# Kernel tuning notes

Hardware: AMD Instinct MI355X
Metric: run time of the kernel (lower is better)

Reference implementation:

```python
import jax, jax.numpy as jnp
from jax import lax
import numpy as np

EPS = 1e-5
NEG_SLOPE = 0.1
POOL = 2


def _cond_block(x, w, b, fcw, fcb, g, be, rm, rv):
    """CondConv1d(k=3,pad=1,num_experts=e) + BatchNorm1d(eval) + LeakyReLU(0.1).
    x: (B, Cin, W); w: (E, Cout, Cin, 3); b: (E, Cout); fcw: (E, Cin); fcb: (E,)
    """
    # routing: adaptive avg pool to 1 -> fc -> sigmoid  => (B, E)
    r = jax.nn.sigmoid(x.mean(axis=-1) @ fcw.T + fcb)
    # per-sample mixed weights/bias
    cw = jnp.einsum('be,eoik->boik', r, w)          # (B, Cout, Cin, 3)
    cb = r @ b                                      # (B, Cout)
    # batched per-sample conv1d (same padding, stride 1)
    def one(xi, wi):
        return lax.conv_general_dilated(
            xi[None], wi, window_strides=(1,), padding=[(1, 1)],
            dimension_numbers=('NCH', 'OIH', 'NCH'))[0]
    y = jax.vmap(one)(x, cw) + cb[:, :, None]       # (B, Cout, W)
    # BatchNorm1d in eval mode (running stats)
    y = (y - rm[None, :, None]) * (g[None, :, None] / jnp.sqrt(rv[None, :, None] + EPS)) + be[None, :, None]
    # LeakyReLU(0.1)
    return jnp.where(y >= 0, y, NEG_SLOPE * y)


def setup_inputs() -> dict:
    key = jax.random.key(0)
    ks = jax.random.split(key, 16)
    B, W = 32, 2048
    chans = [64, 128, 256]
    E = 1  # num_experts default
    inp = {'x': jax.random.normal(ks[0], (B, chans[0], W), dtype=jnp.float32)}
    i = 1
    for li, (ci, co) in enumerate(zip(chans[:-1], chans[1:]), start=1):
        fan_in = ci * 3
        wb = float(np.sqrt(6.0 / fan_in))  # kaiming_uniform a=sqrt(5) scale approx
        bb = float(1.0 / np.sqrt(fan_in))
        inp[f'w{li}'] = jax.random.uniform(ks[i], (E, co, ci, 3), minval=-wb, maxval=wb, dtype=jnp.float32); i += 1
        inp[f'b{li}'] = jax.random.uniform(ks[i], (E, co), minval=-bb, maxval=bb, dtype=jnp.float32); i += 1
        inp[f'fcw{li}'] = jax.random.normal(ks[i], (E, ci), dtype=jnp.float32) * 0.05; i += 1
        inp[f'fcb{li}'] = jnp.zeros((E,), dtype=jnp.float32)
        inp[f'g{li}'] = 1.0 + 0.1 * jax.random.normal(ks[i], (co,), dtype=jnp.float32); i += 1
        inp[f'be{li}'] = 0.1 * jax.random.normal(ks[i], (co,), dtype=jnp.float32); i += 1
        inp[f'rm{li}'] = 0.1 * jax.random.normal(ks[i], (co,), dtype=jnp.float32); i += 1
        inp[f'rv{li}'] = 0.5 + jax.random.uniform(ks[i], (co,), dtype=jnp.float32); i += 1
    return inp


def reference(x, w1, b1, fcw1, fcb1, g1, be1, rm1, rv1,
              w2, b2, fcw2, fcb2, g2, be2, rm2, rv2):
    y = _cond_block(x, w1, b1, fcw1, fcb1, g1, be1, rm1, rv1)
    y = _cond_block(y, w2, b2, fcw2, fcb2, g2, be2, rm2, rv2)
    # max_pool1d(kernel=stride=POOL)
    B, C, W = y.shape
    y = y.reshape(B, C, W // POOL, POOL).max(axis=-1)
    # dropout: eval mode -> identity
    return y
```

## Files before the change

kernel.cpp:

```cpp
#include <hip/hip_runtime.h>
#include <hip/hip_bf16.h>
#include <math.h>

#define BATCH 32
#define WLEN  2048

typedef __attribute__((ext_vector_type(8))) short short8;
typedef __attribute__((ext_vector_type(4))) short short4v;
typedef __attribute__((ext_vector_type(4))) float floatx4;

__device__ inline short f2bf(float f) {
  unsigned u = __float_as_uint(f);
  unsigned r = (u + 0x7fffu + ((u >> 16) & 1u)) >> 16;
  return (short)r;
}

__global__ __launch_bounds__(256) void fused_prep(
    const float* __restrict__ w1, const float* __restrict__ w2,
    const float* __restrict__ x, const float* __restrict__ fcw1,
    short* __restrict__ wp1, short* __restrict__ wp2,
    float* __restrict__ racc1) {
  const int blk = blockIdx.x;
  const int tid = threadIdx.x;
  if (blk < 12) {
    int iw = blk * 256 + tid;
    int o = iw & 127;
    int t = iw >> 7;
    int ig = t & 7;
    int k = t >> 3;
    short8 v;
#pragma unroll
    for (int e = 0; e < 8; ++e) v[e] = f2bf(w1[(o * 64 + ig * 8 + e) * 3 + k]);
    *(short8*)(wp1 + (size_t)iw * 8) = v;
  } else if (blk < 60) {
    int iw = (blk - 12) * 256 + tid;
    int o = iw & 255;
    int t = iw >> 8;
    int ig = t & 15;
    int k = t >> 4;
    short8 v;
#pragma unroll
    for (int e = 0; e < 8; ++e) v[e] = f2bf(w2[(o * 128 + ig * 8 + e) * 3 + k]);
    *(short8*)(wp2 + (size_t)iw * 8) = v;
  } else {
    int t = blk - 60;
    int j = t & 7, b = t >> 3;
    const float4* xb = (const float4*)(x + ((size_t)b * 64 + j * 8) * WLEN);
    float sum = 0.f;
    for (int idx = tid; idx < 8 * 512; idx += 256) {
      int c = idx >> 9;
      float4 v = xb[idx];
      sum += (v.x + v.y + v.z + v.w) * fcw1[j * 8 + c];
    }
    __shared__ float red[256];
    red[tid] = sum;
    __syncthreads();
    for (int s = 128; s > 0; s >>= 1) {
      if (tid < s) red[tid] += red[tid + s];
      __syncthreads();
    }
    if (tid == 0) racc1[b * 8 + j] = red[0];
  }
}

__global__ __launch_bounds__(512, 4) void conv1_mfma(
    const float* __restrict__ x, const short* __restrict__ wp1,
    const float* __restrict__ bias, const float* __restrict__ g,
    const float* __restrict__ be, const float* __restrict__ rm,
    const float* __restrict__ rv, const float* __restrict__ racc1,
    const float* __restrict__ fcb, const float* __restrict__ fcw2,
    short* __restrict__ y1p, float* __restrict__ racc2) {
  const int b = blockIdx.y;
  const int w0 = blockIdx.x * 128;
  const int tid = threadIdx.x;
  const int wave = tid >> 6, lane = tid & 63;
  const int ln = lane & 15, kg = lane >> 4;
  const int oh = wave & 1, wq = wave >> 1;

  __shared__ short xs[8 * 130 * 8];
  __shared__ float red[512];

  const float* xb = x + (size_t)b * 64 * WLEN;
  for (int idx = tid; idx < 8 * 130; idx += 512) {
    int ig = idx / 130;
    int p = idx - ig * 130;
    int w = w0 - 1 + p;
    short8 v = {0, 0, 0, 0, 0, 0, 0, 0};
    if ((unsigned)w < (unsigned)WLEN) {
      const float* src = xb + (size_t)(ig * 8) * WLEN + w;
#pragma unroll
      for (int e = 0; e < 8; ++e) v[e] = f2bf(src[(size_t)e * WLEN]);
    }
    *(short8*)(xs + idx * 8) = v;
  }
  __syncthreads();

  floatx4 acc[4][2];
#pragma unroll
  for (int ms = 0; ms < 4; ++ms)
#pragma unroll
    for (int ns = 0; ns < 2; ++ns) acc[ms][ns] = (floatx4){0.f, 0.f, 0.f, 0.f};

#pragma unroll
  for (int q = 0; q < 2; ++q) {
#pragma unroll
    for (int k = 0; k < 3; ++k) {
      short8 af[4], bf[2];
      const short* wk =
          wp1 + ((size_t)(k * 8 + q * 4 + kg) * 128 + oh * 64 + ln) * 8;
#pragma unroll
      for (int ms = 0; ms < 4; ++ms)
        af[ms] = *(const short8*)(wk + (size_t)ms * 16 * 8);
#pragma unroll
      for (int ns = 0; ns < 2; ++ns)
        bf[ns] = *(const short8*)(
            xs + ((q * 4 + kg) * 130 + wq * 32 + ns * 16 + ln + k) * 8);
#pragma unroll
      for (int ms = 0; ms < 4; ++ms)
#pragma unroll
        for (int ns = 0; ns < 2; ++ns)
          acc[ms][ns] = __builtin_amdgcn_mfma_f32_16x16x32_bf16(
              af[ms], bf[ns], acc[ms][ns], 0, 0, 0);
    }
  }

  float zs = 0.f;
#pragma unroll
  for (int qq = 0; qq < 8; ++qq) zs += racc1[b * 8 + qq];
  float z = zs * (1.f / (float)WLEN) + fcb[0];
  float r1v = 1.f / (1.f + expf(-z));

  float rsum2 = 0.f;
#pragma unroll
  for (int ms = 0; ms < 4; ++ms) {
    const int o0 = oh * 64 + ms * 16 + kg * 4;
    float a_[4], c_[4], fw[4];
#pragma unroll
    for (int rr = 0; rr < 4; ++rr) {
      int o = o0 + rr;
      float s = g[o] * rsqrtf(rv[o] + 1e-5f);
      a_[rr] = r1v * s;
      c_[rr] = (r1v * bias[o] - rm[o]) * s + be[o];
      fw[rr] = fcw2[o];
    }
#pragma unroll
    for (int ns = 0; ns < 2; ++ns) {
      int w = w0 + wq * 32 + ns * 16 + ln;
      short pk[4];
#pragma unroll
      for (int rr = 0; rr < 4; ++rr) {
        float v = acc[ms][ns][rr] * a_[rr] + c_[rr];
        v = v >= 0.f ? v : 0.1f * v;
        rsum2 += v * fw[rr];
        pk[rr] = f2bf(v);
      }
      unsigned u0 = (unsigned)(unsigned short)pk[0] |
                    ((unsigned)(unsigned short)pk[1] << 16);
      unsigned u1 = (unsigned)(unsigned short)pk[2] |
                    ((unsigned)(unsigned short)pk[3] << 16);
      unsigned p0 = __shfl_xor((int)u0, 16);
      unsigned p1 = __shfl_xor((int)u1, 16);
      if (!(kg & 1)) {
        int4 s8;
        s8.x = (int)u0; s8.y = (int)u1; s8.z = (int)p0; s8.w = (int)p1;
        *(int4*)(y1p + ((size_t)(b * 16 + (o0 >> 3)) * WLEN + w) * 8) = s8;
      }
    }
  }
  red[tid] = rsum2;
  __syncthreads();
  for (int s = 256; s > 0; s >>= 1) {
    if (tid < s) red[tid] += red[tid + s];
    __syncthreads();
  }
  if (tid == 0) racc2[b * 16 + blockIdx.x] = red[0];
}

__global__ __launch_bounds__(256) void conv2_mfma(
    const short* __restrict__ y1p, const short* __restrict__ wp2,
    const float* __restrict__ bias, const float* __restrict__ g,
    const float* __restrict__ be, const float* __restrict__ rm,
    const float* __restrict__ rv, const float* __restrict__ racc2,
    const float* __restrict__ fcb, float* __restrict__ out) {
  const int b = blockIdx.y;
  const int w0 = blockIdx.x * 128;
  const int tid = threadIdx.x;
  const int oq = tid >> 6, lane = tid & 63;
  const int ln = lane & 15, kg = lane >> 4;

  __shared__ short xs[16 * 130 * 8];

  const short* yb = y1p + (size_t)b * 16 * WLEN * 8;
  for (int idx = tid; idx < 16 * 130; idx += 256) {
    int ig = idx / 130;
    int p = idx - ig * 130;
    int w = w0 - 1 + p;
    short8 v = {0, 0, 0, 0, 0, 0, 0, 0};
    if ((unsigned)w < (unsigned)WLEN)
      v = *(const short8*)(yb + ((size_t)ig * WLEN + w) * 8);
    *(short8*)(xs + idx * 8) = v;
  }
  __syncthreads();

  floatx4 acc[4][8];
#pragma unroll
  for (int ms = 0; ms < 4; ++ms)
#pragma unroll
    for (int ns = 0; ns < 8; ++ns) acc[ms][ns] = (floatx4){0.f, 0.f, 0.f, 0.f};

#pragma unroll
  for (int c = 0; c < 12; ++c) {
    const int q = c >> 2, kk = c & 3;
    const int qq = c / 3, k = c % 3;
    (void)q; (void)kk;

    short8 af[4], bf[8];
    const short* wk =
        wp2 + ((size_t)(k * 16 + qq * 4 + kg) * 256 + oq * 64 + ln) * 8;
#pragma unroll
    for (int ms = 0; ms < 4; ++ms)
      af[ms] = *(const short8*)(wk + (size_t)ms * 16 * 8);
#pragma unroll
    for (int ns = 0; ns < 8; ++ns)
      bf[ns] = *(const short8*)(
          xs + ((qq * 4 + kg) * 130 + ns * 16 + ln + k) * 8);
#pragma unroll
    for (int ms = 0; ms < 4; ++ms)
#pragma unroll
      for (int ns = 0; ns < 8; ++ns)
        acc[ms][ns] = __builtin_amdgcn_mfma_f32_16x16x32_bf16(
            af[ms], bf[ns], acc[ms][ns], 0, 0, 0);
  }

  float zs = 0.f;
#pragma unroll
  for (int t = 0; t < 16; ++t) zs += racc2[b * 16 + t];
  float z = zs * (1.f / (float)WLEN) + fcb[0];
  float r2v = 1.f / (1.f + expf(-z));

#pragma unroll
  for (int ms = 0; ms < 4; ++ms) {
    const int o0 = oq * 64 + ms * 16 + kg * 4;
    float a_[4], c_[4];
#pragma unroll
    for (int rr = 0; rr < 4; ++rr) {
      int o = o0 + rr;
      float s = g[o] * rsqrtf(rv[o] + 1e-5f);
      a_[rr] = r2v * s;
      c_[rr] = (r2v * bias[o] - rm[o]) * s + be[o];
    }
#pragma unroll
    for (int np = 0; np < 4; ++np) {
      float m0[4], m1[4];
#pragma unroll
      for (int half = 0; half < 2; ++half) {
        int ns = np * 2 + half;
#pragma unroll
        for (int rr = 0; rr < 4; ++rr) {
          float v = acc[ms][ns][rr] * a_[rr] + c_[rr];
          v = v >= 0.f ? v : 0.1f * v;
          float m = fmaxf(v, __shfl_xor(v, 1));
          if (half == 0) m0[rr] = m; else m1[rr] = m;
        }
      }
      const int pc = (w0 >> 1) + np * 16 + ln;
#pragma unroll
      for (int rr = 0; rr < 4; ++rr) {
        int src = kg * 16 + ((ln & 7) << 1);
        float aa = __shfl(m0[rr], src);
        float bb = __shfl(m1[rr], src);
        float val = (ln < 8) ? aa : bb;
        out[((size_t)(b * 256 + o0 + rr)) * (WLEN / 2) + pc] = val;
      }
    }
  }
}

extern "C" void kernel_launch(void* const* d_in, const int* in_sizes, int n_in,
                              void* d_out, int out_size, void* d_ws, size_t ws_size,
                              hipStream_t stream) {
  const float* x    = (const float*)d_in[0];
  const float* w1   = (const float*)d_in[1];
  const float* b1   = (const float*)d_in[2];
  const float* fcw1 = (const float*)d_in[3];
  const float* fcb1 = (const float*)d_in[4];
  const float* g1   = (const float*)d_in[5];
  const float* be1  = (const float*)d_in[6];
  const float* rm1  = (const float*)d_in[7];
  const float* rv1  = (const float*)d_in[8];
  const float* w2   = (const float*)d_in[9];
  const float* b2   = (const float*)d_in[10];
  const float* fcw2 = (const float*)d_in[11];
  const float* fcb2 = (const float*)d_in[12];
  const float* g2   = (const float*)d_in[13];
  const float* be2  = (const float*)d_in[14];
  const float* rm2  = (const float*)d_in[15];
  const float* rv2  = (const float*)d_in[16];
  float* out = (float*)d_out;

  char* ws = (char*)d_ws;
  short* y1p   = (short*)ws;
  short* wp1   = (short*)(ws + (size_t)16 * 1024 * 1024);
  short* wp2   = (short*)(ws + (size_t)16 * 1024 * 1024 + 65536);
  float* racc1 = (float*)(ws + (size_t)16 * 1024 * 1024 + 327680);
  float* racc2 = racc1 + 256;

  fused_prep<<<316, 256, 0, stream>>>(w1, w2, x, fcw1, wp1, wp2, racc1);
  conv1_mfma<<<dim3(16, 32), 512, 0, stream>>>(
      x, wp1, b1, g1, be1, rm1, rv1, racc1, fcb1, fcw2, y1p, racc2);
  conv2_mfma<<<dim3(16, 32), 256, 0, stream>>>(
      y1p, wp2, b2, g2, be2, rm2, rv2, racc2, fcb2, out);
}
```

Baseline: 60.11 us.

## Halve conv2 width tile, load halo via global_load_lds, double grid

conv2 now covers 64 positions per block instead of 128, launching twice as many blocks (1024) with a launch-bounds occupancy hint of 4. The input staging uses direct global-to-LDS loads in two 36-wide sub-tiles, with no bounds checks. The halo at the sequence edges is zeroed afterwards, and the workspace is offset by 4 KB so out-of-range reads stay inside the allocation. The aim is better occupancy and parallelism with cheaper staging, at the cost of fewer accumulators per wave and more weight reloads per output.

```diff
diff --git a/kernel.cpp b/kernel.cpp
--- a/kernel.cpp
+++ b/kernel.cpp
@@ -8,6 +8,11 @@
 typedef __attribute__((ext_vector_type(8))) short short8;
 typedef __attribute__((ext_vector_type(4))) short short4v;
 typedef __attribute__((ext_vector_type(4))) float floatx4;
+
+#define GLOAD_LDS16(g, l)                                                     \
+  __builtin_amdgcn_global_load_lds(                                           \
+      (const __attribute__((address_space(1))) unsigned int*)(g),             \
+      (__attribute__((address_space(3))) unsigned int*)(l), 16, 0, 0)
 
 __device__ inline short f2bf(float f) {
   unsigned u = __float_as_uint(f);
@@ -176,60 +181,82 @@
   if (tid == 0) racc2[b * 16 + blockIdx.x] = red[0];
 }
 
-__global__ __launch_bounds__(256) void conv2_mfma(
+__global__ __launch_bounds__(256, 4) void conv2_mfma(
     const short* __restrict__ y1p, const short* __restrict__ wp2,
     const float* __restrict__ bias, const float* __restrict__ g,
     const float* __restrict__ be, const float* __restrict__ rm,
     const float* __restrict__ rv, const float* __restrict__ racc2,
     const float* __restrict__ fcb, float* __restrict__ out) {
   const int b = blockIdx.y;
-  const int w0 = blockIdx.x * 128;
+  const int w0 = blockIdx.x * 64;
   const int tid = threadIdx.x;
   const int oq = tid >> 6, lane = tid & 63;
   const int ln = lane & 15, kg = lane >> 4;
 
-  __shared__ short xs[16 * 130 * 8];
+  __shared__ short8 xs8[2][576];
+  short* xs[2] = {(short*)xs8[0], (short*)xs8[1]};
 
   const short* yb = y1p + (size_t)b * 16 * WLEN * 8;
-  for (int idx = tid; idx < 16 * 130; idx += 256) {
-    int ig = idx / 130;
-    int p = idx - ig * 130;
-    int w = w0 - 1 + p;
-    short8 v = {0, 0, 0, 0, 0, 0, 0, 0};
-    if ((unsigned)w < (unsigned)WLEN)
-      v = *(const short8*)(yb + ((size_t)ig * WLEN + w) * 8);
-    *(short8*)(xs + idx * 8) = v;
+#pragma unroll
+  for (int u = 0; u < 2; ++u) {
+    const int wu = w0 + u * 32 - 1;
+#pragma unroll
+    for (int base = 0; base < 512; base += 256) {
+      int idx = base + tid;
+      int ig = idx / 36, p = idx - (idx / 36) * 36;
+      GLOAD_LDS16(yb + ((size_t)ig * WLEN + (wu + p)) * 8,
+                  (short*)xs8[u] + (size_t)idx * 8);
+    }
+    if (tid < 64) {
+      int idx = 512 + tid;
+      int ig = idx / 36, p = idx - (idx / 36) * 36;
+      GLOAD_LDS16(yb + ((size_t)ig * WLEN + (wu + p)) * 8,
+                  (short*)xs8[u] + (size_t)idx * 8);
+    }
   }
   __syncthreads();
 
-  floatx4 acc[4][8];
+  if (blockIdx.x == 0 && tid < 16)
+    *(short8*)((short*)xs8[0] + (size_t)(tid * 36 + 0) * 8) = (short8){0,0,0,0,0,0,0,0};
+  if (blockIdx.x == 31 && tid >= 64 && tid < 80)
+    *(short8*)((short*)xs8[1] + (size_t)((tid - 64) * 36 + 33) * 8) = (short8){0,0,0,0,0,0,0,0};
+  __syncthreads();
+
+  floatx4 acc[4][2][2];
 #pragma unroll
   for (int ms = 0; ms < 4; ++ms)
 #pragma unroll
-    for (int ns = 0; ns < 8; ++ns) acc[ms][ns] = (floatx4){0.f, 0.f, 0.f, 0.f};
+    for (int u = 0; u < 2; ++u)
+#pragma unroll
+      for (int ns = 0; ns < 2; ++ns) acc[ms][u][ns] = (floatx4){0.f, 0.f, 0.f, 0.f};
 
 #pragma unroll
   for (int c = 0; c < 12; ++c) {
-    const int q = c >> 2, kk = c & 3;
     const int qq = c / 3, k = c % 3;
-    (void)q; (void)kk;
-
-    short8 af[4], bf[8];
+
+    short8 af[4];
     const short* wk =
         wp2 + ((size_t)(k * 16 + qq * 4 + kg) * 256 + oq * 64 + ln) * 8;
 #pragma unroll
     for (int ms = 0; ms < 4; ++ms)
       af[ms] = *(const short8*)(wk + (size_t)ms * 16 * 8);
-#pragma unroll
-    for (int ns = 0; ns < 8; ++ns)
-      bf[ns] = *(const short8*)(
-          xs + ((qq * 4 + kg) * 130 + ns * 16 + ln + k) * 8);
+
+    short8 bf[2][2];
+#pragma unroll
+    for (int u = 0; u < 2; ++u)
+#pragma unroll
+      for (int ns = 0; ns < 2; ++ns)
+        bf[u][ns] = *(const short8*)(
+            (short*)xs8[u] + (size_t)((qq * 4 + kg) * 36 + ns * 16 + ln + k) * 8);
+
 #pragma unroll
     for (int ms = 0; ms < 4; ++ms)
 #pragma unroll
-      for (int ns = 0; ns < 8; ++ns)
-        acc[ms][ns] = __builtin_amdgcn_mfma_f32_16x16x32_bf16(
-            af[ms], bf[ns], acc[ms][ns], 0, 0, 0);
+      for (int u = 0; u < 2; ++u)
+#pragma unroll
+        for (int ns = 0; ns < 2; ++ns)
+          acc[ms][u][ns] = __builtin_amdgcn_mfma_f32_16x16x32_bf16(
+              af[ms], bf[u][ns], acc[ms][u][ns], 0, 0, 0);
   }
 
   float zs = 0.f;
@@ -250,20 +277,19 @@
       c_[rr] = (r2v * bias[o] - rm[o]) * s + be[o];
     }
 #pragma unroll
-    for (int np = 0; np < 4; ++np) {
+    for (int u = 0; u < 2; ++u) {
       float m0[4], m1[4];
 #pragma unroll
       for (int half = 0; half < 2; ++half) {
-        int ns = np * 2 + half;
 #pragma unroll
         for (int rr = 0; rr < 4; ++rr) {
-          float v = acc[ms][ns][rr] * a_[rr] + c_[rr];
+          float v = acc[ms][u][half][rr] * a_[rr] + c_[rr];
           v = v >= 0.f ? v : 0.1f * v;
           float m = fmaxf(v, __shfl_xor(v, 1));
           if (half == 0) m0[rr] = m; else m1[rr] = m;
         }
       }
-      const int pc = (w0 >> 1) + np * 16 + ln;
+      const int pc = (w0 >> 1) + u * 16 + ln;
 #pragma unroll
       for (int rr = 0; rr < 4; ++rr) {
         int src = kg * 16 + ((ln & 7) << 1);
@@ -299,15 +325,15 @@
   float* out = (float*)d_out;
 
   char* ws = (char*)d_ws;
-  short* y1p   = (short*)ws;
-  short* wp1   = (short*)(ws + (size_t)16 * 1024 * 1024);
-  short* wp2   = (short*)(ws + (size_t)16 * 1024 * 1024 + 65536);
-  float* racc1 = (float*)(ws + (size_t)16 * 1024 * 1024 + 327680);
+  short* y1p   = (short*)(ws + 4096);
+  short* wp1   = (short*)(ws + 4096 + (size_t)16 * 1024 * 1024);
+  short* wp2   = (short*)(ws + 4096 + (size_t)16 * 1024 * 1024 + 65536);
+  float* racc1 = (float*)(ws + (size_t)17 * 1024 * 1024);
   float* racc2 = racc1 + 256;
 
   fused_prep<<<316, 256, 0, stream>>>(w1, w2, x, fcw1, wp1, wp2, racc1);
   conv1_mfma<<<dim3(16, 32), 512, 0, stream>>>(
       x, wp1, b1, g1, be1, rm1, rv1, racc1, fcb1, fcw2, y1p, racc2);
-  conv2_mfma<<<dim3(16, 32), 256, 0, stream>>>(
+  conv2_mfma<<<dim3(32, 32), 256, 0, stream>>>(
       y1p, wp2, b2, g2, be2, rm2, rv2, racc2, fcb2, out);
 }
```

After: 56.08 us. 6.7% less time.

## Split conv2 across output-channel halves with more waves; stage conv1 weights in LDS

Applied to the files above, without the earlier changes.

conv2 now launches twice as many blocks, each covering half the output channels with 8 waves. Every wave holds a 4x2 accumulator tile instead of 4x8, which cuts register pressure and raises occupancy and parallelism. The cost is that each block loads the same y1 tile again, doubling reads of the input activations. conv1 now copies its whole bf16 weight matrix into LDS with global_load_lds and reads the MFMA A-fragments from shared memory instead of global memory. The LDS copy relies on the existing __syncthreads that follows the x staging.

```diff
diff --git a/kernel.cpp b/kernel.cpp
--- a/kernel.cpp
+++ b/kernel.cpp
@@ -8,6 +8,11 @@
 typedef __attribute__((ext_vector_type(8))) short short8;
 typedef __attribute__((ext_vector_type(4))) short short4v;
 typedef __attribute__((ext_vector_type(4))) float floatx4;
+
+#define GLOAD_LDS16(g, l)                                                     \
+  __builtin_amdgcn_global_load_lds(                                           \
+      (const __attribute__((address_space(1))) unsigned int*)(g),             \
+      (__attribute__((address_space(3))) unsigned int*)(l), 16, 0, 0)
 
 __device__ inline short f2bf(float f) {
   unsigned u = __float_as_uint(f);
@@ -77,8 +82,15 @@
   const int ln = lane & 15, kg = lane >> 4;
   const int oh = wave & 1, wq = wave >> 1;
 
+  __shared__ short wl[3 * 8 * 128 * 8];
   __shared__ short xs[8 * 130 * 8];
   __shared__ float red[512];
+
+#pragma unroll
+  for (int c = 0; c < 6; ++c) {
+    const int ib = c * 512 + wave * 64;
+    GLOAD_LDS16(wp1 + (size_t)(ib + lane) * 8, wl + (size_t)ib * 8);
+  }
 
   const float* xb = x + (size_t)b * 64 * WLEN;
   for (int idx = tid; idx < 8 * 130; idx += 512) {
@@ -106,8 +118,7 @@
 #pragma unroll
     for (int k = 0; k < 3; ++k) {
       short8 af[4], bf[2];
-      const short* wk =
-          wp1 + ((size_t)(k * 8 + q * 4 + kg) * 128 + oh * 64 + ln) * 8;
+      const short* wk = wl + ((size_t)(k * 8 + q * 4 + kg) * 128 + oh * 64 + ln) * 8;
 #pragma unroll
       for (int ms = 0; ms < 4; ++ms)
         af[ms] = *(const short8*)(wk + (size_t)ms * 16 * 8);
@@ -176,7 +187,7 @@
   if (tid == 0) racc2[b * 16 + blockIdx.x] = red[0];
 }
 
-__global__ __launch_bounds__(256) void conv2_mfma(
+__global__ __launch_bounds__(512, 4) void conv2_mfma(
     const short* __restrict__ y1p, const short* __restrict__ wp2,
     const float* __restrict__ bias, const float* __restrict__ g,
     const float* __restrict__ be, const float* __restrict__ rm,
@@ -184,14 +195,16 @@
     const float* __restrict__ fcb, float* __restrict__ out) {
   const int b = blockIdx.y;
   const int w0 = blockIdx.x * 128;
+  const int ohh = blockIdx.z;
   const int tid = threadIdx.x;
-  const int oq = tid >> 6, lane = tid & 63;
+  const int wave = tid >> 6, lane = tid & 63;
   const int ln = lane & 15, kg = lane >> 4;
+  const int oq2 = wave & 1, wq = wave >> 1;
 
   __shared__ short xs[16 * 130 * 8];
 
   const short* yb = y1p + (size_t)b * 16 * WLEN * 8;
-  for (int idx = tid; idx < 16 * 130; idx += 256) {
+  for (int idx = tid; idx < 16 * 130; idx += 512) {
     int ig = idx / 130;
     int p = idx - ig * 130;
     int w = w0 - 1 + p;
@@ -202,32 +215,29 @@
   }
   __syncthreads();
 
-  floatx4 acc[4][8];
+  floatx4 acc[4][2];
 #pragma unroll
   for (int ms = 0; ms < 4; ++ms)
 #pragma unroll
-    for (int ns = 0; ns < 8; ++ns) acc[ms][ns] = (floatx4){0.f, 0.f, 0.f, 0.f};
+    for (int ns = 0; ns < 2; ++ns) acc[ms][ns] = (floatx4){0.f, 0.f, 0.f, 0.f};
 
 #pragma unroll
   for (int c = 0; c < 12; ++c) {
-    const int q = c >> 2, kk = c & 3;
-    const int qq = c / 3, k = c % 3;
-    (void)q; (void)kk;
-
-    short8 af[4], bf[8];
-    const short* wk =
-        wp2 + ((size_t)(k * 16 + qq * 4 + kg) * 256 + oq * 64 + ln) * 8;
+    const int q = c / 3, k = c % 3;
+    short8 af[4], bf[2];
+    const short* wk = wp2 + ((size_t)(k * 16 + q * 4 + kg) * 256 +
+                             ohh * 128 + oq2 * 64 + ln) * 8;
 #pragma unroll
     for (int ms = 0; ms < 4; ++ms)
       af[ms] = *(const short8*)(wk + (size_t)ms * 16 * 8);
 #pragma unroll
-    for (int ns = 0; ns < 8; ++ns)
+    for (int ns = 0; ns < 2; ++ns)
       bf[ns] = *(const short8*)(
-          xs + ((qq * 4 + kg) * 130 + ns * 16 + ln + k) * 8);
+          xs + ((q * 4 + kg) * 130 + wq * 32 + ns * 16 + ln + k) * 8);
 #pragma unroll
     for (int ms = 0; ms < 4; ++ms)
 #pragma unroll
-      for (int ns = 0; ns < 8; ++ns)
+      for (int ns = 0; ns < 2; ++ns)
         acc[ms][ns] = __builtin_amdgcn_mfma_f32_16x16x32_bf16(
             af[ms], bf[ns], acc[ms][ns], 0, 0, 0);
   }
@@ -240,7 +250,7 @@
 
 #pragma unroll
   for (int ms = 0; ms < 4; ++ms) {
-    const int o0 = oq * 64 + ms * 16 + kg * 4;
+    const int o0 = ohh * 128 + oq2 * 64 + ms * 16 + kg * 4;
     float a_[4], c_[4];
 #pragma unroll
     for (int rr = 0; rr < 4; ++rr) {
@@ -249,29 +259,25 @@
       a_[rr] = r2v * s;
       c_[rr] = (r2v * bias[o] - rm[o]) * s + be[o];
     }
-#pragma unroll
-    for (int np = 0; np < 4; ++np) {
-      float m0[4], m1[4];
-#pragma unroll
-      for (int half = 0; half < 2; ++half) {
-        int ns = np * 2 + half;
-#pragma unroll
-        for (int rr = 0; rr < 4; ++rr) {
-          float v = acc[ms][ns][rr] * a_[rr] + c_[rr];
-          v = v >= 0.f ? v : 0.1f * v;
-          float m = fmaxf(v, __shfl_xor(v, 1));
-          if (half == 0) m0[rr] = m; else m1[rr] = m;
-        }
+    float m0[4], m1[4];
+#pragma unroll
+    for (int half = 0; half < 2; ++half) {
+#pragma unroll
+      for (int rr = 0; rr < 4; ++rr) {
+        float v = acc[ms][half][rr] * a_[rr] + c_[rr];
+        v = v >= 0.f ? v : 0.1f * v;
+        float m = fmaxf(v, __shfl_xor(v, 1));
+        if (half == 0) m0[rr] = m; else m1[rr] = m;
       }
-      const int pc = (w0 >> 1) + np * 16 + ln;
-#pragma unroll
-      for (int rr = 0; rr < 4; ++rr) {
-        int src = kg * 16 + ((ln & 7) << 1);
-        float aa = __shfl(m0[rr], src);
-        float bb = __shfl(m1[rr], src);
-        float val = (ln < 8) ? aa : bb;
-        out[((size_t)(b * 256 + o0 + rr)) * (WLEN / 2) + pc] = val;
-      }
+    }
+    const int pc = (w0 >> 1) + wq * 16 + ln;
+#pragma unroll
+    for (int rr = 0; rr < 4; ++rr) {
+      int src = kg * 16 + ((ln & 7) << 1);
+      float aa = __shfl(m0[rr], src);
+      float bb = __shfl(m1[rr], src);
+      float val = (ln < 8) ? aa : bb;
+      out[((size_t)(b * 256 + o0 + rr)) * (WLEN / 2) + pc] = val;
     }
   }
 }
@@ -308,6 +314,6 @@
   fused_prep<<<316, 256, 0, stream>>>(w1, w2, x, fcw1, wp1, wp2, racc1);
   conv1_mfma<<<dim3(16, 32), 512, 0, stream>>>(
       x, wp1, b1, g1, be1, rm1, rv1, racc1, fcb1, fcw2, y1p, racc2);
-  conv2_mfma<<<dim3(16, 32), 256, 0, stream>>>(
+  conv2_mfma<<<dim3(16, 32, 2), 512, 0, stream>>>(
       y1p, wp2, b2, g2, be2, rm2, rv2, racc2, fcb2, out);
 }
```

After: 55.57 us. 7.6% less time.
